# Optimization experiments

Measured on AMD Instinct MI355X. Metric: run time of the kernel, lower is better.

## Reference

```python
import jax, jax.numpy as jnp
import numpy as np


def setup_inputs() -> dict:
    key = jax.random.key(0)
    k1, k2 = jax.random.split(key)
    B, H, S, D = 1, 8, 4096, 64
    CHUNK = 256
    N = S // CHUNK  # 16 chunks
    q = jax.random.normal(k1, (B, H, S, D), dtype=jnp.float32)
    kv_quad_state = jax.random.normal(k2, (B, H, N, D, D, D), dtype=jnp.float32)
    return {"q": q, "kv_quad_state": kv_quad_state}


def reference(q, kv_quad_state):
    # O = 0.5 * einsum('bhndef,bhncd,bhnce->bhncf', S, Q_scaled, Q_scaled)
    # where Q is scaled by head_dim**-0.5 and chunked along seq.
    b, h, s, d = q.shape
    n = kv_quad_state.shape[2]
    c = s // n  # chunk_size
    q_scale = jnp.asarray(d, q.dtype) ** -0.5
    qc = (q * q_scale).reshape(b, h, n, c, d)  # (b,h,n,c,d)
    # pairwise contraction: first Q@S over d -> (b,h,n,c,e,f), then weight by Q_ce, sum e
    tmp = jnp.einsum('bhncd,bhndef->bhncef', qc, kv_quad_state)
    out = 0.5 * jnp.einsum('bhnce,bhncef->bhncf', qc, tmp)
    return out.reshape(b, h, s, d)
```

## Files before the change

### kernel.cpp

```cpp
#include <hip/hip_runtime.h>
#include <hip/hip_bf16.h>

typedef __attribute__((ext_vector_type(4))) float f32x4;
typedef __attribute__((ext_vector_type(8))) short bf16x8;
typedef __attribute__((ext_vector_type(4))) short bf16x4;

#define QS_STRIDE 68
#define BT_STRIDE 72

__device__ __forceinline__ short f2bf(float x) {
    __hip_bfloat16 h = __float2bfloat16(x);
    return __builtin_bit_cast(short, h);
}

#define FENCE() do {                                         \
    asm volatile("s_waitcnt lgkmcnt(0)" ::: "memory");       \
    __builtin_amdgcn_s_barrier();                            \
    asm volatile("" ::: "memory");                           \
} while (0)

__global__ __launch_bounds__(256, 2) void quad_form_kernel(
    const float* __restrict__ q, const float* __restrict__ kv, float* __restrict__ out)
{
    __shared__ float qs[64 * QS_STRIDE];
    __shared__ __align__(16) unsigned short Bt[2][64 * BT_STRIDE];

    const int tid = threadIdx.x;

    const int wg = blockIdx.x;
    const int xcd = wg & 7, p = wg >> 3;
    const int chunk = xcd * 16 + (p >> 2);
    const int quarter = p & 3;

    const float* qch = q   + (size_t)chunk * (256 * 64) + quarter * (64 * 64);
    const float* Sch = kv  + (size_t)chunk * 262144;
    float*       och = out + (size_t)chunk * (256 * 64) + quarter * (64 * 64);

#pragma unroll
    for (int i = 0; i < 4; ++i) {
        int idx4 = i * 256 + tid;
        int row = idx4 >> 4;
        int col = (idx4 & 15) << 2;
        f32x4 v = *(const f32x4*)(qch + idx4 * 4);
        v *= 0.125f;
        *(f32x4*)&qs[row * QS_STRIDE + col] = v;
    }

    const int fS = tid & 63;
    const int kq = tid >> 6;
    const float* Sptr = Sch + fS + kq * (16 * 64);

    float r0[16], r1[16];

    auto issue = [&](float* r, int d0) {
        const float* p0 = Sptr + d0 * 4096;
#pragma unroll
        for (int i = 0; i < 16; ++i)
            r[i] = p0[i * 64];
    };
    auto stage = [&](const float* r, int buf) {
        unsigned short* base = &Bt[buf][fS * BT_STRIDE + kq * 16];
#pragma unroll
        for (int i4 = 0; i4 < 4; ++i4) {
            bf16x4 wv;
#pragma unroll
            for (int j = 0; j < 4; ++j) wv[j] = f2bf(r[i4 * 4 + j]);
            *(bf16x4*)(base + i4 * 4) = wv;
        }
    };

    const int lane = tid & 63;
    const int w = tid >> 6;
    const int ra = lane & 15;
    const int kg = lane >> 4;

    f32x4 acc[4] = {};
    const float* qrow = qs + (w * 16 + ra) * QS_STRIDE;

    auto mfma_phase = [&](int buf, int d0) {
        float s0 = qrow[d0];
#pragma unroll
        for (int Ks = 0; Ks < 2; ++Ks) {
            int e0 = Ks * 32 + kg * 8;
            f32x4 u0 = *(const f32x4*)(qrow + e0);
            f32x4 u1 = *(const f32x4*)(qrow + e0 + 4);
            bf16x8 a;
#pragma unroll
            for (int j = 0; j < 4; ++j) {
                a[j]     = f2bf(s0 * u0[j]);
                a[j + 4] = f2bf(s0 * u1[j]);
            }
#pragma unroll
            for (int Nt = 0; Nt < 4; ++Nt) {
                bf16x8 b = *(const bf16x8*)&Bt[buf][(Nt * 16 + ra) * BT_STRIDE + e0];
                acc[Nt] = __builtin_amdgcn_mfma_f32_16x16x32_bf16(a, b, acc[Nt], 0, 0, 0);
            }
        }
    };

    issue(r0, 0); issue(r1, 1);
    stage(r0, 0);
    issue(r0, 2);
    FENCE();

    for (int i = 0; i < 64; i += 2) {
        stage(r1, 1);
        if (i + 3 < 64) issue(r1, i + 3);
        mfma_phase(0, i);
        FENCE();

        if (i + 2 < 64) {
            stage(r0, 0);
            if (i + 4 < 64) issue(r0, i + 4);
        }
        mfma_phase(1, i + 1);
        FENCE();
    }

#pragma unroll
    for (int Nt = 0; Nt < 4; ++Nt)
#pragma unroll
        for (int j = 0; j < 4; ++j) {
            int r = w * 16 + kg * 4 + j;
            och[r * 64 + Nt * 16 + ra] = 0.5f * acc[Nt][j];
        }
}

extern "C" void kernel_launch(void* const* d_in, const int* in_sizes, int n_in,
                              void* d_out, int out_size, void* d_ws, size_t ws_size,
                              hipStream_t stream) {
    const float* q  = (const float*)d_in[0];
    const float* kv = (const float*)d_in[1];
    float* out = (float*)d_out;
    hipLaunchKernelGGL(quad_form_kernel, dim3(512), dim3(256), 0, stream, q, kv, out);
}
```

Before: 47.88 us.

## Use 2x2 wave tiling, hoist Q row fragments, and triple-buffer S prefetch registers

Each wave now computes a 32x32 output tile (2x2 MFMA tiles) instead of a 16x64 strip, so each B fragment read from LDS feeds two MFMAs. The Q row fragments used to build the A operand are loaded once into registers instead of being reread from LDS every phase. Global prefetch of S slices goes three deep through three register buffers. This adds register pressure under launch bounds of two blocks per CU, and the loop is a non-unrolled rotation of three phases.

Result: no change. 47.52 us (-0.7%).

```diff
diff --git a/kernel.cpp b/kernel.cpp
--- a/kernel.cpp
+++ b/kernel.cpp
@@ -8,7 +8,7 @@
 #define QS_STRIDE 68
 #define BT_STRIDE 72
 
-__device__ __forceinline__ short f2bf(float x) {
+static __device__ __forceinline__ short f2bf(float x) {
     __hip_bfloat16 h = __float2bfloat16(x);
     return __builtin_bit_cast(short, h);
 }
@@ -32,15 +32,14 @@
     const int chunk = xcd * 16 + (p >> 2);
     const int quarter = p & 3;
 
-    const float* qch = q   + (size_t)chunk * (256 * 64) + quarter * (64 * 64);
+    const float* qch = q   + (size_t)chunk * 16384 + quarter * 4096;
     const float* Sch = kv  + (size_t)chunk * 262144;
-    float*       och = out + (size_t)chunk * (256 * 64) + quarter * (64 * 64);
+    float*       och = out + (size_t)chunk * 16384 + quarter * 4096;
 
 #pragma unroll
     for (int i = 0; i < 4; ++i) {
         int idx4 = i * 256 + tid;
-        int row = idx4 >> 4;
-        int col = (idx4 & 15) << 2;
+        int row = idx4 >> 4, col = (idx4 & 15) << 2;
         f32x4 v = *(const f32x4*)(qch + idx4 * 4);
         v *= 0.125f;
         *(f32x4*)&qs[row * QS_STRIDE + col] = v;
@@ -48,9 +47,9 @@
 
     const int fS = tid & 63;
     const int kq = tid >> 6;
-    const float* Sptr = Sch + fS + kq * (16 * 64);
+    const float* Sptr = Sch + fS + kq * 1024;
 
-    float r0[16], r1[16];
+    float r0[16], r1[16], r2[16];
 
     auto issue = [&](float* r, int d0) {
         const float* p0 = Sptr + d0 * 4096;
@@ -71,59 +70,78 @@
 
     const int lane = tid & 63;
     const int w = tid >> 6;
-    const int ra = lane & 15;
-    const int kg = lane >> 4;
+    const int wm = w & 1, wn = w >> 1;
+    const int ra = lane & 15, kg = lane >> 4;
 
-    f32x4 acc[4] = {};
-    const float* qrow = qs + (w * 16 + ra) * QS_STRIDE;
+    f32x4 acc[2][2] = {};
+    const float* qrow0 = qs + (wm * 32 + ra) * QS_STRIDE;
+    const float* qrow1 = qrow0 + 16 * QS_STRIDE;
 
-    auto mfma_phase = [&](int buf, int d0) {
-        float s0 = qrow[d0];
+    issue(r0, 0); issue(r1, 1); issue(r2, 2);
+    stage(r0, 0);
+    issue(r0, 3);
+    FENCE();
+
+    f32x4 u[2][2][2];
+#pragma unroll
+    for (int Mt = 0; Mt < 2; ++Mt) {
+        const float* qr = Mt ? qrow1 : qrow0;
 #pragma unroll
         for (int Ks = 0; Ks < 2; ++Ks) {
-            int e0 = Ks * 32 + kg * 8;
-            f32x4 u0 = *(const f32x4*)(qrow + e0);
-            f32x4 u1 = *(const f32x4*)(qrow + e0 + 4);
-            bf16x8 a;
+            u[Mt][Ks][0] = *(const f32x4*)(qr + Ks * 32 + kg * 8);
+            u[Mt][Ks][1] = *(const f32x4*)(qr + Ks * 32 + kg * 8 + 4);
+        }
+    }
+    float s0c = qrow0[0], s1c = qrow1[0];
+
+    auto mfma_phase = [&](int buf, float s0, float s1) {
+#pragma unroll
+        for (int Ks = 0; Ks < 2; ++Ks) {
+            const int e0 = Ks * 32 + kg * 8;
+            bf16x8 a0, a1;
 #pragma unroll
             for (int j = 0; j < 4; ++j) {
-                a[j]     = f2bf(s0 * u0[j]);
-                a[j + 4] = f2bf(s0 * u1[j]);
+                a0[j]     = f2bf(s0 * u[0][Ks][0][j]);
+                a0[j + 4] = f2bf(s0 * u[0][Ks][1][j]);
+                a1[j]     = f2bf(s1 * u[1][Ks][0][j]);
+                a1[j + 4] = f2bf(s1 * u[1][Ks][1][j]);
             }
 #pragma unroll
-            for (int Nt = 0; Nt < 4; ++Nt) {
-                bf16x8 b = *(const bf16x8*)&Bt[buf][(Nt * 16 + ra) * BT_STRIDE + e0];
-                acc[Nt] = __builtin_amdgcn_mfma_f32_16x16x32_bf16(a, b, acc[Nt], 0, 0, 0);
+            for (int Nt = 0; Nt < 2; ++Nt) {
+                bf16x8 b = *(const bf16x8*)&Bt[buf][(wn * 32 + Nt * 16 + ra) * BT_STRIDE + e0];
+                acc[0][Nt] = __builtin_amdgcn_mfma_f32_16x16x32_bf16(a0, b, acc[0][Nt], 0, 0, 0);
+                acc[1][Nt] = __builtin_amdgcn_mfma_f32_16x16x32_bf16(a1, b, acc[1][Nt], 0, 0, 0);
             }
         }
     };
 
-    issue(r0, 0); issue(r1, 1);
-    stage(r0, 0);
-    issue(r0, 2);
-    FENCE();
+    int i = 0;
+    auto phase = [&](float* rb) {
+        stage(rb, (i + 1) & 1);
+        if (i + 4 < 64) issue(rb, i + 4);
+        mfma_phase(i & 1, s0c, s1c);
+        float ns0 = qrow0[i + 1], ns1 = qrow1[i + 1];
+        FENCE();
+        s0c = ns0; s1c = ns1;
+        ++i;
+    };
 
-    for (int i = 0; i < 64; i += 2) {
-        stage(r1, 1);
-        if (i + 3 < 64) issue(r1, i + 3);
-        mfma_phase(0, i);
-        FENCE();
-
-        if (i + 2 < 64) {
-            stage(r0, 0);
-            if (i + 4 < 64) issue(r0, i + 4);
-        }
-        mfma_phase(1, i + 1);
-        FENCE();
+#pragma unroll 1
+    for (int it = 0; it < 21; ++it) {
+        phase(r1); phase(r2); phase(r0);
     }
+    mfma_phase(1, s0c, s1c);
 
 #pragma unroll
-    for (int Nt = 0; Nt < 4; ++Nt)
+    for (int Mt = 0; Mt < 2; ++Mt)
 #pragma unroll
-        for (int j = 0; j < 4; ++j) {
-            int r = w * 16 + kg * 4 + j;
-            och[r * 64 + Nt * 16 + ra] = 0.5f * acc[Nt][j];
-        }
+        for (int Nt = 0; Nt < 2; ++Nt)
+#pragma unroll
+            for (int j = 0; j < 4; ++j) {
+                int r = wm * 32 + Mt * 16 + kg * 4 + j;
+                int c = wn * 32 + Nt * 16 + ra;
+                och[r * 64 + c] = 0.5f * acc[Mt][Nt][j];
+            }
 }
 
 extern "C" void kernel_launch(void* const* d_in, const int* in_sizes, int n_in,
```

## Split work by output column slice instead of row quarter to cut redundant S reads

Applied to the files above, without the earlier changes.

Each workgroup now handles all 256 rows of a chunk for a 16-column slice of f, instead of 64 rows for all 64 columns. It therefore reads only a quarter of the chunk's kv state rather than the whole chunk four times over. The full scaled Q chunk is kept in LDS and the Q fragments are cached in registers. Two d-slices are staged per pipeline step, and each B fragment is reused across four M tiles. In exchange, LDS use rises sharply, global loads become narrower 64-byte segments, and the A fragments are recomputed for every MFMA.

New measurement: 48.58 us. Within noise of the previous version (+1.5%).

```diff
diff --git a/kernel.cpp b/kernel.cpp
--- a/kernel.cpp
+++ b/kernel.cpp
@@ -7,8 +7,9 @@
 
 #define QS_STRIDE 68
 #define BT_STRIDE 72
+#define SLICE_B   (16 * BT_STRIDE)
 
-__device__ __forceinline__ short f2bf(float x) {
+static __device__ __forceinline__ short f2bf(float x) {
     __hip_bfloat16 h = __float2bfloat16(x);
     return __builtin_bit_cast(short, h);
 }
@@ -22,107 +23,118 @@
 __global__ __launch_bounds__(256, 2) void quad_form_kernel(
     const float* __restrict__ q, const float* __restrict__ kv, float* __restrict__ out)
 {
-    __shared__ float qs[64 * QS_STRIDE];
-    __shared__ __align__(16) unsigned short Bt[2][64 * BT_STRIDE];
+    __shared__ float qs[256 * QS_STRIDE];
+    __shared__ __align__(16) unsigned short Bt[2][2 * SLICE_B];
 
     const int tid = threadIdx.x;
 
     const int wg = blockIdx.x;
     const int xcd = wg & 7, p = wg >> 3;
     const int chunk = xcd * 16 + (p >> 2);
-    const int quarter = p & 3;
+    const int f0 = (p & 3) * 16;
 
-    const float* qch = q   + (size_t)chunk * (256 * 64) + quarter * (64 * 64);
-    const float* Sch = kv  + (size_t)chunk * 262144;
-    float*       och = out + (size_t)chunk * (256 * 64) + quarter * (64 * 64);
+    const float* qch = q   + (size_t)chunk * 16384;
+    const float* Sch = kv  + (size_t)chunk * 262144 + f0;
+    float*       och = out + (size_t)chunk * 16384 + f0;
 
 #pragma unroll
-    for (int i = 0; i < 4; ++i) {
+    for (int i = 0; i < 16; ++i) {
         int idx4 = i * 256 + tid;
-        int row = idx4 >> 4;
-        int col = (idx4 & 15) << 2;
+        int row = idx4 >> 4, col = (idx4 & 15) << 2;
         f32x4 v = *(const f32x4*)(qch + idx4 * 4);
         v *= 0.125f;
         *(f32x4*)&qs[row * QS_STRIDE + col] = v;
     }
 
-    const int fS = tid & 63;
-    const int kq = tid >> 6;
-    const float* Sptr = Sch + fS + kq * (16 * 64);
+    const int fT = tid & 15;
+    const int eg = tid >> 4;
+    const float* Sptr = Sch + fT + eg * 4 * 64;
 
-    float r0[16], r1[16];
+    float rA[8], rB[8];
 
     auto issue = [&](float* r, int d0) {
-        const float* p0 = Sptr + d0 * 4096;
+        const float* pa = Sptr + d0 * 4096;
+        const float* pb = pa + 4096;
 #pragma unroll
-        for (int i = 0; i < 16; ++i)
-            r[i] = p0[i * 64];
+        for (int i = 0; i < 4; ++i) { r[i] = pa[i * 64]; r[4 + i] = pb[i * 64]; }
     };
     auto stage = [&](const float* r, int buf) {
-        unsigned short* base = &Bt[buf][fS * BT_STRIDE + kq * 16];
+        unsigned short* base = &Bt[buf][fT * BT_STRIDE + eg * 4];
+        bf16x4 w0, w1;
 #pragma unroll
-        for (int i4 = 0; i4 < 4; ++i4) {
-            bf16x4 wv;
-#pragma unroll
-            for (int j = 0; j < 4; ++j) wv[j] = f2bf(r[i4 * 4 + j]);
-            *(bf16x4*)(base + i4 * 4) = wv;
-        }
+        for (int j = 0; j < 4; ++j) { w0[j] = f2bf(r[j]); w1[j] = f2bf(r[4 + j]); }
+        *(bf16x4*)base = w0;
+        *(bf16x4*)(base + SLICE_B) = w1;
     };
 
     const int lane = tid & 63;
     const int w = tid >> 6;
-    const int ra = lane & 15;
-    const int kg = lane >> 4;
+    const int ra = lane & 15, kg = lane >> 4;
 
     f32x4 acc[4] = {};
-    const float* qrow = qs + (w * 16 + ra) * QS_STRIDE;
+    const float* qrow[4];
+#pragma unroll
+    for (int Mt = 0; Mt < 4; ++Mt) qrow[Mt] = qs + (w * 64 + Mt * 16 + ra) * QS_STRIDE;
 
-    auto mfma_phase = [&](int buf, int d0) {
-        float s0 = qrow[d0];
+    issue(rA, 0); issue(rB, 2);
+    stage(rA, 0);
+    issue(rA, 4);
+    FENCE();
+
+    f32x4 u[4][2][2];
+#pragma unroll
+    for (int Mt = 0; Mt < 4; ++Mt)
 #pragma unroll
         for (int Ks = 0; Ks < 2; ++Ks) {
-            int e0 = Ks * 32 + kg * 8;
-            f32x4 u0 = *(const f32x4*)(qrow + e0);
-            f32x4 u1 = *(const f32x4*)(qrow + e0 + 4);
-            bf16x8 a;
+            u[Mt][Ks][0] = *(const f32x4*)(qrow[Mt] + Ks * 32 + kg * 8);
+            u[Mt][Ks][1] = *(const f32x4*)(qrow[Mt] + Ks * 32 + kg * 8 + 4);
+        }
+
+    auto mfma_pair = [&](int buf, int d0) {
 #pragma unroll
-            for (int j = 0; j < 4; ++j) {
-                a[j]     = f2bf(s0 * u0[j]);
-                a[j + 4] = f2bf(s0 * u1[j]);
-            }
+        for (int sl = 0; sl < 2; ++sl) {
+            float s[4];
 #pragma unroll
-            for (int Nt = 0; Nt < 4; ++Nt) {
-                bf16x8 b = *(const bf16x8*)&Bt[buf][(Nt * 16 + ra) * BT_STRIDE + e0];
-                acc[Nt] = __builtin_amdgcn_mfma_f32_16x16x32_bf16(a, b, acc[Nt], 0, 0, 0);
+            for (int Mt = 0; Mt < 4; ++Mt) s[Mt] = qrow[Mt][d0 + sl];
+#pragma unroll
+            for (int Ks = 0; Ks < 2; ++Ks) {
+                bf16x8 b = *(const bf16x8*)&Bt[buf][sl * SLICE_B + ra * BT_STRIDE + Ks * 32 + kg * 8];
+#pragma unroll
+                for (int Mt = 0; Mt < 4; ++Mt) {
+                    bf16x8 a;
+#pragma unroll
+                    for (int j = 0; j < 4; ++j) {
+                        a[j]     = f2bf(s[Mt] * u[Mt][Ks][0][j]);
+                        a[j + 4] = f2bf(s[Mt] * u[Mt][Ks][1][j]);
+                    }
+                    acc[Mt] = __builtin_amdgcn_mfma_f32_16x16x32_bf16(a, b, acc[Mt], 0, 0, 0);
+                }
             }
         }
     };
 
-    issue(r0, 0); issue(r1, 1);
-    stage(r0, 0);
-    issue(r0, 2);
-    FENCE();
-
-    for (int i = 0; i < 64; i += 2) {
-        stage(r1, 1);
-        if (i + 3 < 64) issue(r1, i + 3);
-        mfma_phase(0, i);
+#pragma unroll 1
+    for (int it = 0; it < 16; ++it) {
+        const int d = it * 4;
+        stage(rB, 1);
+        if (d + 6 < 64) issue(rB, d + 6);
+        mfma_pair(0, d);
         FENCE();
 
-        if (i + 2 < 64) {
-            stage(r0, 0);
-            if (i + 4 < 64) issue(r0, i + 4);
+        if (d + 4 < 64) {
+            stage(rA, 0);
+            if (d + 8 < 64) issue(rA, d + 8);
         }
-        mfma_phase(1, i + 1);
-        FENCE();
+        mfma_pair(1, d + 2);
+        if (it < 15) FENCE();
     }
 
 #pragma unroll
-    for (int Nt = 0; Nt < 4; ++Nt)
+    for (int Mt = 0; Mt < 4; ++Mt)
 #pragma unroll
         for (int j = 0; j < 4; ++j) {
-            int r = w * 16 + kg * 4 + j;
-            och[r * 64 + Nt * 16 + ra] = 0.5f * acc[Nt][j];
+            int r = w * 64 + Mt * 16 + kg * 4 + j;
+            och[r * 64 + ra] = 0.5f * acc[Mt][j];
         }
 }
 
```

## Drop LDS staging, keep Q in registers, switch to fp16 MFMA with half-chunk tiles

Applied to the files above, without the earlier changes.

Restructures the kernel so each workgroup handles half a chunk (128 rows) instead of a quarter. Each wave owns a 16-column slice of f and reads S directly from global memory into registers. This removes the LDS staging and barriers. The scaled Q fragments are precomputed once into registers as fp16 and multiplied per d by an fp16 splat of q[d], using fp16 MFMA with round-toward-zero conversions. The grid halves to 256 blocks with launch bounds of 1, which trades occupancy and fp16 range and precision for fewer global S reads per row and no shared-memory synchronisation.

Result: slower. 52.49 us (+9.6%).

```diff
diff --git a/kernel.cpp b/kernel.cpp
--- a/kernel.cpp
+++ b/kernel.cpp
@@ -1,129 +1,105 @@
 #include <hip/hip_runtime.h>
-#include <hip/hip_bf16.h>
+#include <hip/hip_fp16.h>
 
 typedef __attribute__((ext_vector_type(4))) float f32x4;
-typedef __attribute__((ext_vector_type(8))) short bf16x8;
-typedef __attribute__((ext_vector_type(4))) short bf16x4;
+typedef __attribute__((ext_vector_type(8))) _Float16 f16x8;
+typedef __attribute__((ext_vector_type(2))) _Float16 f16x2;
+typedef __attribute__((ext_vector_type(2))) __fp16 fp16x2_raw;
 
-#define QS_STRIDE 68
-#define BT_STRIDE 72
+union F16X8 { f16x2 p[4]; f16x8 w; };
 
-__device__ __forceinline__ short f2bf(float x) {
-    __hip_bfloat16 h = __float2bfloat16(x);
-    return __builtin_bit_cast(short, h);
+static __device__ __forceinline__ f16x2 pkrtz(float a, float b) {
+    fp16x2_raw r = __builtin_amdgcn_cvt_pkrtz(a, b);
+    return __builtin_bit_cast(f16x2, r);
 }
 
-#define FENCE() do {                                         \
-    asm volatile("s_waitcnt lgkmcnt(0)" ::: "memory");       \
-    __builtin_amdgcn_s_barrier();                            \
-    asm volatile("" ::: "memory");                           \
+#define LOADB(BUF, dd) do {                                             \
+    const float* _p = Sb + (dd) * 4096;                                 \
+    _Pragma("unroll") for (int _K = 0; _K < 2; ++_K)                    \
+    _Pragma("unroll") for (int _j = 0; _j < 8; ++_j)                    \
+        b##BUF[_K][_j] = _p[_K * 2048 + _j * 64];                       \
+    const float* _q = qsp + (dd);                                       \
+    _Pragma("unroll") for (int _M = 0; _M < 8; ++_M)                    \
+        s##BUF[_M] = _q[_M * 1024];                                     \
 } while (0)
 
-__global__ __launch_bounds__(256, 2) void quad_form_kernel(
+#define COMPUTE(BUF) do {                                               \
+    f16x8 _bb[2];                                                       \
+    _Pragma("unroll") for (int _K = 0; _K < 2; ++_K) {                  \
+        F16X8 _bu;                                                      \
+        _Pragma("unroll") for (int _h = 0; _h < 4; ++_h)                \
+            _bu.p[_h] = pkrtz(b##BUF[_K][2 * _h], b##BUF[_K][2 * _h + 1]); \
+        _bb[_K] = _bu.w;                                                \
+    }                                                                   \
+    _Pragma("unroll") for (int _M = 0; _M < 8; ++_M) {                  \
+        float _sf = 0.125f * s##BUF[_M];                                \
+        f16x2 _sh = pkrtz(_sf, _sf);                                    \
+        _Pragma("unroll") for (int _K = 0; _K < 2; ++_K) {              \
+            F16X8 _au;                                                  \
+            _Pragma("unroll") for (int _h = 0; _h < 4; ++_h)            \
+                _au.p[_h] = _sh * u[_M][_K][_h];                        \
+            acc[_M] = __builtin_amdgcn_mfma_f32_16x16x32_f16(_au.w, _bb[_K], acc[_M], 0, 0, 0); \
+        }                                                               \
+    }                                                                   \
+} while (0)
+
+__global__ __launch_bounds__(256, 1) void quad_form_kernel(
     const float* __restrict__ q, const float* __restrict__ kv, float* __restrict__ out)
 {
-    __shared__ float qs[64 * QS_STRIDE];
-    __shared__ __align__(16) unsigned short Bt[2][64 * BT_STRIDE];
-
     const int tid = threadIdx.x;
 
     const int wg = blockIdx.x;
     const int xcd = wg & 7, p = wg >> 3;
-    const int chunk = xcd * 16 + (p >> 2);
-    const int quarter = p & 3;
-
-    const float* qch = q   + (size_t)chunk * (256 * 64) + quarter * (64 * 64);
-    const float* Sch = kv  + (size_t)chunk * 262144;
-    float*       och = out + (size_t)chunk * (256 * 64) + quarter * (64 * 64);
-
-#pragma unroll
-    for (int i = 0; i < 4; ++i) {
-        int idx4 = i * 256 + tid;
-        int row = idx4 >> 4;
-        int col = (idx4 & 15) << 2;
-        f32x4 v = *(const f32x4*)(qch + idx4 * 4);
-        v *= 0.125f;
-        *(f32x4*)&qs[row * QS_STRIDE + col] = v;
-    }
-
-    const int fS = tid & 63;
-    const int kq = tid >> 6;
-    const float* Sptr = Sch + fS + kq * (16 * 64);
-
-    float r0[16], r1[16];
-
-    auto issue = [&](float* r, int d0) {
-        const float* p0 = Sptr + d0 * 4096;
-#pragma unroll
-        for (int i = 0; i < 16; ++i)
-            r[i] = p0[i * 64];
-    };
-    auto stage = [&](const float* r, int buf) {
-        unsigned short* base = &Bt[buf][fS * BT_STRIDE + kq * 16];
-#pragma unroll
-        for (int i4 = 0; i4 < 4; ++i4) {
-            bf16x4 wv;
-#pragma unroll
-            for (int j = 0; j < 4; ++j) wv[j] = f2bf(r[i4 * 4 + j]);
-            *(bf16x4*)(base + i4 * 4) = wv;
-        }
-    };
+    const int chunk = xcd * 16 + (p >> 1);
+    const int chalf = p & 1;
 
     const int lane = tid & 63;
     const int w = tid >> 6;
-    const int ra = lane & 15;
-    const int kg = lane >> 4;
+    const int ra = lane & 15, kg = lane >> 4;
+    const int f0 = w * 16;
 
-    f32x4 acc[4] = {};
-    const float* qrow = qs + (w * 16 + ra) * QS_STRIDE;
+    const float* qch = q   + (size_t)chunk * 16384 + chalf * 8192;
+    const float* Sch = kv  + (size_t)chunk * 262144;
+    float*       och = out + (size_t)chunk * 16384 + chalf * 8192;
 
-    auto mfma_phase = [&](int buf, int d0) {
-        float s0 = qrow[d0];
+    const float* Sb  = Sch + kg * 512 + f0 + ra;
+    const float* qsp = qch + ra * 64;
+
+    f16x2 u[8][2][4];
+#pragma unroll
+    for (int Mt = 0; Mt < 8; ++Mt)
 #pragma unroll
         for (int Ks = 0; Ks < 2; ++Ks) {
-            int e0 = Ks * 32 + kg * 8;
-            f32x4 u0 = *(const f32x4*)(qrow + e0);
-            f32x4 u1 = *(const f32x4*)(qrow + e0 + 4);
-            bf16x8 a;
-#pragma unroll
-            for (int j = 0; j < 4; ++j) {
-                a[j]     = f2bf(s0 * u0[j]);
-                a[j + 4] = f2bf(s0 * u1[j]);
-            }
-#pragma unroll
-            for (int Nt = 0; Nt < 4; ++Nt) {
-                bf16x8 b = *(const bf16x8*)&Bt[buf][(Nt * 16 + ra) * BT_STRIDE + e0];
-                acc[Nt] = __builtin_amdgcn_mfma_f32_16x16x32_bf16(a, b, acc[Nt], 0, 0, 0);
-            }
+            const float* qr = qch + (Mt * 16 + ra) * 64 + Ks * 32 + kg * 8;
+            f32x4 g0 = *(const f32x4*)qr;
+            f32x4 g1 = *(const f32x4*)(qr + 4);
+            u[Mt][Ks][0] = pkrtz(0.125f * g0[0], 0.125f * g0[1]);
+            u[Mt][Ks][1] = pkrtz(0.125f * g0[2], 0.125f * g0[3]);
+            u[Mt][Ks][2] = pkrtz(0.125f * g1[0], 0.125f * g1[1]);
+            u[Mt][Ks][3] = pkrtz(0.125f * g1[2], 0.125f * g1[3]);
         }
-    };
 
-    issue(r0, 0); issue(r1, 1);
-    stage(r0, 0);
-    issue(r0, 2);
-    FENCE();
+    f32x4 acc[8] = {};
+    float bA[2][8], bB[2][8];
+    float sA[8], sB[8];
 
-    for (int i = 0; i < 64; i += 2) {
-        stage(r1, 1);
-        if (i + 3 < 64) issue(r1, i + 3);
-        mfma_phase(0, i);
-        FENCE();
-
-        if (i + 2 < 64) {
-            stage(r0, 0);
-            if (i + 4 < 64) issue(r0, i + 4);
-        }
-        mfma_phase(1, i + 1);
-        FENCE();
+    LOADB(A, 0);
+    LOADB(B, 1);
+#pragma unroll 1
+    for (int d = 0; d < 62; d += 2) {
+        COMPUTE(A);
+        LOADB(A, d + 2);
+        COMPUTE(B);
+        LOADB(B, d + 3);
     }
+    COMPUTE(A);
+    COMPUTE(B);
 
 #pragma unroll
-    for (int Nt = 0; Nt < 4; ++Nt)
+    for (int Mt = 0; Mt < 8; ++Mt)
 #pragma unroll
-        for (int j = 0; j < 4; ++j) {
-            int r = w * 16 + kg * 4 + j;
-            och[r * 64 + Nt * 16 + ra] = 0.5f * acc[Nt][j];
-        }
+        for (int j = 0; j < 4; ++j)
+            och[(Mt * 16 + kg * 4 + j) * 64 + f0 + ra] = 0.5f * acc[Mt][j];
 }
 
 extern "C" void kernel_launch(void* const* d_in, const int* in_sizes, int n_in,
@@ -132,5 +108,5 @@
     const float* q  = (const float*)d_in[0];
     const float* kv = (const float*)d_in[1];
     float* out = (float*)d_out;
-    hipLaunchKernelGGL(quad_form_kernel, dim3(512), dim3(256), 0, stream, q, kv, out);
+    hipLaunchKernelGGL(quad_form_kernel, dim3(256), dim3(256), 0, stream, q, kv, out);
 }
```
